# Performance work log

Hardware: AMD Instinct MI355X
Metric: run time of the kernel (lower is better)

## Reference

```python
import jax, jax.numpy as jnp
import numpy as np

NEG_SLOPE = 0.01  # F.leaky_relu default


def gcn_layer(h_in, W, b, src, dst, deg_inv_sqrt, n_nodes):
    # GCNConv: linear transform, then symmetric-normalized sum aggregation
    # with self-loops (PyG gcn_norm with add_self_loops=True).
    h = h_in @ W                                   # [N, F_out]
    norm = deg_inv_sqrt[src] * deg_inv_sqrt[dst]   # [E]
    agg = jax.ops.segment_sum(norm[:, None] * h[src], dst, num_segments=n_nodes)
    agg = agg + (deg_inv_sqrt * deg_inv_sqrt)[:, None] * h  # self-loop term (norm = 1/deg)
    return agg + b


def setup_inputs() -> dict:
    key = jax.random.key(0)
    ks = jax.random.split(key, 10)
    N, E = 100000, 3200000
    F_in, H, C = 512, 256, 64
    x = jax.random.normal(ks[0], (N, F_in), dtype=jnp.float32)
    edge_index = jax.random.randint(ks[1], (2, E), 0, N, dtype=jnp.int32)
    dims = [(F_in, H), (H, H), (H, H), (H, C)]
    params = {}
    for i, (fi, fo) in enumerate(dims):
        scale = (1.0 / fi) ** 0.5
        params[f"W{i}"] = jax.random.normal(ks[2 + i], (fi, fo), dtype=jnp.float32) * scale
        params[f"b{i}"] = jnp.zeros((fo,), dtype=jnp.float32)
    return {"x": x, "edge_index": edge_index, **params}


def reference(x, edge_index, W0, b0, W1, b1, W2, b2, W3, b3):
    N = x.shape[0]
    src, dst = edge_index[0], edge_index[1]
    # degree including self-loop (edge weights all 1)
    deg = jax.ops.segment_sum(jnp.ones_like(src, dtype=x.dtype), dst, num_segments=N) + 1.0
    deg_inv_sqrt = jax.lax.rsqrt(deg)
    Ws = [W0, W1, W2, W3]
    bs = [b0, b1, b2, b3]
    h = x
    for i in range(4):
        h = gcn_layer(h, Ws[i], bs[i], src, dst, deg_inv_sqrt, N)
        if i != 3:
            h = jax.nn.leaky_relu(h, NEG_SLOPE)
    return jax.nn.softmax(h, axis=1)
```

## Files before the change

kernel.cpp:

```cpp
#include <hip/hip_runtime.h>
#include <hip/hip_fp16.h>


#define NEG_SLOPE 0.01f

typedef __attribute__((ext_vector_type(8))) _Float16 f16x8;
typedef __attribute__((ext_vector_type(4))) float f32x4;

__device__ inline f16x8 f16x8_zero() {
    f16x8 v;
#pragma unroll
    for (int q = 0; q < 8; ++q) v[q] = (_Float16)0.f;
    return v;
}

__global__ void k_degree(const int* __restrict__ dst, int* __restrict__ cnt, int E) {
    int i = blockIdx.x * 256 + threadIdx.x;
    if (i < E) atomicAdd(&cnt[dst[i]], 1);
}

__global__ void k_dis(const int* __restrict__ cnt, float* __restrict__ dis, int N) {
    int i = blockIdx.x * 256 + threadIdx.x;
    if (i < N) dis[i] = rsqrtf((float)cnt[i] + 1.0f);
}

__global__ void k_scan1(const int* __restrict__ cnt, int* __restrict__ excl,
                        int* __restrict__ partials, int n) {
    __shared__ int tmp[1024];
    int tid = threadIdx.x;
    int i = blockIdx.x * 1024 + tid;
    int v = (i < n) ? cnt[i] : 0;
    tmp[tid] = v;
    __syncthreads();
    for (int off = 1; off < 1024; off <<= 1) {
        int t = (tid >= off) ? tmp[tid - off] : 0;
        __syncthreads();
        tmp[tid] += t;
        __syncthreads();
    }
    if (i < n) excl[i] = tmp[tid] - v;
    if (tid == 1023) partials[blockIdx.x] = tmp[tid];
}

__global__ void k_scan2(int* __restrict__ partials, int n) {
    __shared__ int tmp[1024];
    int tid = threadIdx.x;
    int v = (tid < n) ? partials[tid] : 0;
    tmp[tid] = v;
    __syncthreads();
    for (int off = 1; off < 1024; off <<= 1) {
        int t = (tid >= off) ? tmp[tid - off] : 0;
        __syncthreads();
        tmp[tid] += t;
        __syncthreads();
    }
    if (tid < n) partials[tid] = tmp[tid] - v;
}

__global__ void k_scan3(int* __restrict__ row_ptr, const int* __restrict__ partials,
                        int* __restrict__ fill_ptr, int n, int E) {
    int i = blockIdx.x * 256 + threadIdx.x;
    if (i < n) {
        int v = row_ptr[i] + partials[i >> 10];
        row_ptr[i] = v;
        fill_ptr[i] = v;
    }
    if (i == n) row_ptr[n] = E;
}

__global__ void k_fill(const int* __restrict__ src, const int* __restrict__ dst,
                       int* __restrict__ fill_ptr, int* __restrict__ csr, int E) {
    int i = blockIdx.x * 256 + threadIdx.x;
    if (i < E) {
        int s = src[i], d = dst[i];
        int p = atomicAdd(&fill_ptr[d], 1);
        csr[p] = s;
    }
}

__global__ void k_convW(const float* __restrict__ W, _Float16* __restrict__ Wt,
                        int K, int Nf) {
    int gid = blockIdx.x * 256 + threadIdx.x;
    if (gid < K * Nf) {
        int n = gid / K, k = gid - n * K;
        Wt[gid] = (_Float16)W[(size_t)k * Nf + n];
    }
}

template <int BN, bool A_HALF, bool OUT_HALF>
__global__ __launch_bounds__(256) void k_gemm_mfma(const void* __restrict__ Ap,
                                                   const _Float16* __restrict__ Bt,
                                                   void* __restrict__ Cp,
                                                   const float* __restrict__ rowscale,
                                                   int M, int K, int Nf) {
    constexpr int BM = 128, BK = 32;
    constexpr int WAVES_N = (BN == 128) ? 2 : 1;
    constexpr int WAVES_M = 4 / WAVES_N;
    constexpr int WM = BM / (WAVES_M * 16);
    constexpr int WN = BN / (WAVES_N * 16);
    constexpr int LDK = BK + 8;
    __shared__ _Float16 As[BM][LDK];
    __shared__ _Float16 Bs[BN][LDK];

    const int tid = threadIdx.x;
    const int ln = tid & 63, wv = tid >> 6;
    const int wm = wv / WAVES_N, wn = wv % WAVES_N;
    const int rowq = wm * WM * 16, colq = wn * WN * 16;
    const int rowBase = blockIdx.x * BM;
    const int colBase = blockIdx.y * BN;
    const int l15 = ln & 15, lq = ln >> 4;

    f32x4 acc[WM][WN];
#pragma unroll
    for (int i = 0; i < WM; ++i)
#pragma unroll
        for (int j = 0; j < WN; ++j) {
            acc[i][j][0] = 0.f; acc[i][j][1] = 0.f;
            acc[i][j][2] = 0.f; acc[i][j][3] = 0.f;
        }

    constexpr int ASL2 = (BM * BK / 8) / 256;
    constexpr int BSL2 = (BN * BK / 8) / 256;

    for (int kt = 0; kt < K; kt += BK) {
        f16x8 aL[ASL2];
        float4 aF[ASL2][2];
#pragma unroll
        for (int s2 = 0; s2 < ASL2; ++s2) {
            int s = tid + s2 * 256;
            int r = s >> 2, k0 = (s & 3) * 8;
            int gr = rowBase + r;
            if constexpr (A_HALF) {
                aL[s2] = (gr < M)
                    ? *(const f16x8*)((const _Float16*)Ap + (size_t)gr * K + kt + k0)
                    : f16x8_zero();
            } else {
                if (gr < M) {
                    const float* ap = (const float*)Ap + (size_t)gr * K + kt + k0;
                    aF[s2][0] = *(const float4*)ap;
                    aF[s2][1] = *(const float4*)(ap + 4);
                } else {
                    aF[s2][0] = make_float4(0.f, 0.f, 0.f, 0.f);
                    aF[s2][1] = make_float4(0.f, 0.f, 0.f, 0.f);
                }
            }
        }
        f16x8 bL[BSL2];
#pragma unroll
        for (int s2 = 0; s2 < BSL2; ++s2) {
            int s = tid + s2 * 256;
            int n = s >> 2, k0 = (s & 3) * 8;
            bL[s2] = *(const f16x8*)&Bt[(size_t)(colBase + n) * K + kt + k0];
        }
        __syncthreads();
#pragma unroll
        for (int s2 = 0; s2 < ASL2; ++s2) {
            int s = tid + s2 * 256;
            int r = s >> 2, k0 = (s & 3) * 8;
            if constexpr (A_HALF) {
                *(f16x8*)&As[r][k0] = aL[s2];
            } else {
                f16x8 h;
                h[0] = (_Float16)aF[s2][0].x; h[1] = (_Float16)aF[s2][0].y;
                h[2] = (_Float16)aF[s2][0].z; h[3] = (_Float16)aF[s2][0].w;
                h[4] = (_Float16)aF[s2][1].x; h[5] = (_Float16)aF[s2][1].y;
                h[6] = (_Float16)aF[s2][1].z; h[7] = (_Float16)aF[s2][1].w;
                *(f16x8*)&As[r][k0] = h;
            }
        }
#pragma unroll
        for (int s2 = 0; s2 < BSL2; ++s2) {
            int s = tid + s2 * 256;
            int n = s >> 2, k0 = (s & 3) * 8;
            *(f16x8*)&Bs[n][k0] = bL[s2];
        }
        __syncthreads();
        f16x8 af[WM], bf[WN];
#pragma unroll
        for (int i = 0; i < WM; ++i)
            af[i] = *(const f16x8*)&As[rowq + i * 16 + l15][lq * 8];
#pragma unroll
        for (int j = 0; j < WN; ++j)
            bf[j] = *(const f16x8*)&Bs[colq + j * 16 + l15][lq * 8];
#pragma unroll
        for (int i = 0; i < WM; ++i)
#pragma unroll
            for (int j = 0; j < WN; ++j)
                acc[i][j] = __builtin_amdgcn_mfma_f32_16x16x32_f16(af[i], bf[j],
                                                                   acc[i][j], 0, 0, 0);
    }

#pragma unroll
    for (int i = 0; i < WM; ++i) {
#pragma unroll
        for (int r = 0; r < 4; ++r) {
            int row = rowBase + rowq + i * 16 + lq * 4 + r;
            if (row < M) {
                float rs = rowscale[row];
#pragma unroll
                for (int j = 0; j < WN; ++j) {
                    int col = colBase + colq + j * 16 + l15;
                    float v = rs * acc[i][j][r];
                    if constexpr (OUT_HALF)
                        ((_Float16*)Cp)[(size_t)row * Nf + col] = (_Float16)v;
                    else
                        ((float*)Cp)[(size_t)row * Nf + col] = v;
                }
            }
        }
    }
}

__global__ __launch_bounds__(256) void k_agg256_h(const float2* __restrict__ H2,
                                                  const int* __restrict__ row_ptr,
                                                  const int* __restrict__ csr,
                                                  const float* __restrict__ dis,
                                                  const float* __restrict__ bias,
                                                  _Float16* __restrict__ out, int N) {
    int wave = threadIdx.x >> 6;
    int lane = threadIdx.x & 63;
    int node = blockIdx.x * 4 + wave;
    if (node >= N) return;
    int beg = row_ptr[node], end = row_ptr[node + 1];
    float ax = 0.f, ay = 0.f, az = 0.f, aw = 0.f;

    int e = beg;
    for (; e + 8 <= end; e += 8) {
        int msrc = csr[e + (lane & 7)];
#pragma unroll
        for (int j = 0; j < 8; ++j) {
            int s = __shfl(msrc, j);
            float2 raw = H2[(size_t)s * 64 + lane];
            float2 f0 = __half22float2(*(const __half2*)&raw.x);
            float2 f1 = __half22float2(*(const __half2*)&raw.y);
            ax += f0.x; ay += f0.y; az += f1.x; aw += f1.y;
        }
    }
    if (e < end) {
        int idx = e + (lane & 7);
        int msrc = csr[idx < end ? idx : end - 1];
        int n = end - e;
#pragma unroll
        for (int j = 0; j < 8; ++j) {
            if (j < n) {
                int s = __shfl(msrc, j);
                float2 raw = H2[(size_t)s * 64 + lane];
                float2 f0 = __half22float2(*(const __half2*)&raw.x);
                float2 f1 = __half22float2(*(const __half2*)&raw.y);
                ax += f0.x; ay += f0.y; az += f1.x; aw += f1.y;
            }
        }
    }

    float di = dis[node];
    float2 raws = H2[(size_t)node * 64 + lane];
    float2 s0 = __half22float2(*(const __half2*)&raws.x);
    float2 s1 = __half22float2(*(const __half2*)&raws.y);
    float4 b  = ((const float4*)bias)[lane];
    float rx = fmaf(di, ax + s0.x, b.x);
    float ry = fmaf(di, ay + s0.y, b.y);
    float rz = fmaf(di, az + s1.x, b.z);
    float rw = fmaf(di, aw + s1.y, b.w);
    rx = rx > 0.f ? rx : NEG_SLOPE * rx;
    ry = ry > 0.f ? ry : NEG_SLOPE * ry;
    rz = rz > 0.f ? rz : NEG_SLOPE * rz;
    rw = rw > 0.f ? rw : NEG_SLOPE * rw;
    _Float16 hh[4] = {(_Float16)rx, (_Float16)ry, (_Float16)rz, (_Float16)rw};
    *(float2*)&out[(size_t)node * 256 + lane * 4] = *(float2*)hh;
}

__global__ __launch_bounds__(256) void k_agg64_softmax(const _Float16* __restrict__ H,
                                                       const int* __restrict__ row_ptr,
                                                       const int* __restrict__ csr,
                                                       const float* __restrict__ dis,
                                                       const float* __restrict__ bias,
                                                       float* __restrict__ out, int N) {
    int wave = threadIdx.x >> 6;
    int lane = threadIdx.x & 63;
    int node = blockIdx.x * 4 + wave;
    if (node >= N) return;
    int beg = row_ptr[node], end = row_ptr[node + 1];
    float acc = 0.f;

    int e = beg;
    for (; e + 8 <= end; e += 8) {
        int msrc = csr[e + (lane & 7)];
#pragma unroll
        for (int j = 0; j < 8; ++j) {
            int s = __shfl(msrc, j);
            acc += (float)H[(size_t)s * 64 + lane];
        }
    }
    if (e < end) {
        int idx = e + (lane & 7);
        int msrc = csr[idx < end ? idx : end - 1];
        int n = end - e;
#pragma unroll
        for (int j = 0; j < 8; ++j) {
            if (j < n) {
                int s = __shfl(msrc, j);
                acc += (float)H[(size_t)s * 64 + lane];
            }
        }
    }

    float di = dis[node];
    float v = fmaf(di, acc + (float)H[(size_t)node * 64 + lane], bias[lane]);
    float m = v;
#pragma unroll
    for (int off = 32; off; off >>= 1) m = fmaxf(m, __shfl_xor(m, off));
    float ex = __expf(v - m);
    float s = ex;
#pragma unroll
    for (int off = 32; off; off >>= 1) s += __shfl_xor(s, off);
    out[(size_t)node * 64 + lane] = ex / s;
}

extern "C" void kernel_launch(void* const* d_in, const int* in_sizes, int n_in,
                              void* d_out, int out_size, void* d_ws, size_t ws_size,
                              hipStream_t stream) {
    const float* x  = (const float*)d_in[0];
    const int*   ei = (const int*)d_in[1];
    const float* W0 = (const float*)d_in[2];
    const float* b0 = (const float*)d_in[3];
    const float* W1 = (const float*)d_in[4];
    const float* b1 = (const float*)d_in[5];
    const float* W2 = (const float*)d_in[6];
    const float* b2 = (const float*)d_in[7];
    const float* W3 = (const float*)d_in[8];
    const float* b3 = (const float*)d_in[9];

    const int N = in_sizes[0] / 512;
    const int E = in_sizes[1] / 2;
    const int* src = ei;
    const int* dst = ei + E;

    auto align256 = [](size_t v) { return (v + 255) & ~(size_t)255; };
    char* w = (char*)d_ws;
    _Float16* hA = (_Float16*)w;     w += align256((size_t)N * 256 * 4);
    _Float16* hB = (_Float16*)w;     w += align256((size_t)N * 256 * 4);
    int*   csr = (int*)w;            w += align256((size_t)E * 4);
    int*   cnt = (int*)w;            w += align256((size_t)N * 4);
    float* dis = (float*)w;          w += align256((size_t)N * 4);
    int*   row_ptr = (int*)w;        w += align256((size_t)(N + 1) * 4);
    int*   fill_ptr = (int*)w;       w += align256((size_t)N * 4);
    int*   partials = (int*)w;       w += align256((size_t)1024 * 4);
    _Float16* Wt0 = (_Float16*)w;    w += align256((size_t)256 * 512 * 2);
    _Float16* Wt1 = (_Float16*)w;    w += align256((size_t)256 * 256 * 2);
    _Float16* Wt2 = (_Float16*)w;    w += align256((size_t)256 * 256 * 2);
    _Float16* Wt3 = (_Float16*)w;    w += align256((size_t)64 * 256 * 2);
    (void)ws_size; (void)n_in; (void)out_size;

    const int nchunks = (N + 1023) / 1024;

    hipMemsetAsync(cnt, 0, (size_t)N * 4, stream);
    k_degree<<<(E + 255) / 256, 256, 0, stream>>>(dst, cnt, E);
    k_dis<<<(N + 255) / 256, 256, 0, stream>>>(cnt, dis, N);
    k_scan1<<<nchunks, 1024, 0, stream>>>(cnt, row_ptr, partials, N);
    k_scan2<<<1, 1024, 0, stream>>>(partials, nchunks);
    k_scan3<<<(N + 1 + 255) / 256, 256, 0, stream>>>(row_ptr, partials, fill_ptr, N, E);
    k_fill<<<(E + 255) / 256, 256, 0, stream>>>(src, dst, fill_ptr, csr, E);

    k_convW<<<(512 * 256 + 255) / 256, 256, 0, stream>>>(W0, Wt0, 512, 256);
    k_convW<<<(256 * 256 + 255) / 256, 256, 0, stream>>>(W1, Wt1, 256, 256);
    k_convW<<<(256 * 256 + 255) / 256, 256, 0, stream>>>(W2, Wt2, 256, 256);
    k_convW<<<(256 * 64 + 255) / 256, 256, 0, stream>>>(W3, Wt3, 256, 64);

    const int gridM = (N + 127) / 128;
    const int nodeBlocks = (N + 3) / 4;

    k_gemm_mfma<128, false, true><<<dim3(gridM, 2), 256, 0, stream>>>(x, Wt0, hA, dis,
                                                                      N, 512, 256);
    k_agg256_h<<<nodeBlocks, 256, 0, stream>>>((const float2*)hA, row_ptr, csr, dis, b0,
                                               hB, N);
    k_gemm_mfma<128, true, true><<<dim3(gridM, 2), 256, 0, stream>>>(hB, Wt1, hA, dis,
                                                                     N, 256, 256);
    k_agg256_h<<<nodeBlocks, 256, 0, stream>>>((const float2*)hA, row_ptr, csr, dis, b1,
                                               hB, N);
    k_gemm_mfma<128, true, true><<<dim3(gridM, 2), 256, 0, stream>>>(hB, Wt2, hA, dis,
                                                                     N, 256, 256);
    k_agg256_h<<<nodeBlocks, 256, 0, stream>>>((const float2*)hA, row_ptr, csr, dis, b2,
                                               hB, N);
    k_gemm_mfma<64, true, true><<<dim3(gridM, 1), 256, 0, stream>>>(hB, Wt3, hA, dis,
                                                                    N, 256, 64);
    k_agg64_softmax<<<nodeBlocks, 256, 0, stream>>>(hA, row_ptr, csr, dis, b3,
                                                    (float*)d_out, N);
}
```

Before: 1.626 ms.

## Build CSR via two-level bucket fill to localize scatter atomics

```diff
diff --git a/kernel.cpp b/kernel.cpp
--- a/kernel.cpp
+++ b/kernel.cpp
@@ -58,23 +58,45 @@
 }
 
 __global__ void k_scan3(int* __restrict__ row_ptr, const int* __restrict__ partials,
-                        int* __restrict__ fill_ptr, int n, int E) {
+                        int n, int E) {
     int i = blockIdx.x * 256 + threadIdx.x;
-    if (i < n) {
-        int v = row_ptr[i] + partials[i >> 10];
-        row_ptr[i] = v;
-        fill_ptr[i] = v;
-    }
+    if (i < n) row_ptr[i] = row_ptr[i] + partials[i >> 10];
     if (i == n) row_ptr[n] = E;
 }
 
-__global__ void k_fill(const int* __restrict__ src, const int* __restrict__ dst,
-                       int* __restrict__ fill_ptr, int* __restrict__ csr, int E) {
+__global__ void k_init_bcur(const int* __restrict__ row_ptr, int* __restrict__ bcur,
+                            int nbuk) {
+    int b = blockIdx.x * 256 + threadIdx.x;
+    if (b < nbuk) bcur[b * 16] = row_ptr[b << 7];
+}
+
+__global__ void k_bucket_fill(const int* __restrict__ src, const int* __restrict__ dst,
+                              int* __restrict__ bcur, int* __restrict__ bpool, int E) {
     int i = blockIdx.x * 256 + threadIdx.x;
     if (i < E) {
         int s = src[i], d = dst[i];
-        int p = atomicAdd(&fill_ptr[d], 1);
-        csr[p] = s;
+        int b = d >> 7;
+        int p = atomicAdd(&bcur[b * 16], 1);
+        bpool[p] = (s << 7) | (d & 127);
+    }
+}
+
+__global__ __launch_bounds__(256) void k_place(const int* __restrict__ bpool,
+                                               const int* __restrict__ row_ptr,
+                                               int* __restrict__ csr, int N) {
+    __shared__ int cur[128];
+    int b = blockIdx.x;
+    int n0 = b << 7;
+    int nn = min(128, N - n0);
+    int tid = threadIdx.x;
+    if (tid < nn) cur[tid] = row_ptr[n0 + tid];
+    __syncthreads();
+    int lo = row_ptr[n0];
+    int hi = row_ptr[n0 + nn];
+    for (int i = lo + tid; i < hi; i += 256) {
+        int e = bpool[i];
+        int p = atomicAdd(&cur[e & 127], 1);
+        csr[p] = e >> 7;
     }
 }
 
@@ -334,16 +356,18 @@
     const int E = in_sizes[1] / 2;
     const int* src = ei;
     const int* dst = ei + E;
+    const int NBUK = (N + 127) >> 7;
 
     auto align256 = [](size_t v) { return (v + 255) & ~(size_t)255; };
     char* w = (char*)d_ws;
-    _Float16* hA = (_Float16*)w;     w += align256((size_t)N * 256 * 4);
-    _Float16* hB = (_Float16*)w;     w += align256((size_t)N * 256 * 4);
+    _Float16* hA = (_Float16*)w;     w += align256((size_t)N * 256 * 2);
+    _Float16* hB = (_Float16*)w;     w += align256((size_t)N * 256 * 2);
     int*   csr = (int*)w;            w += align256((size_t)E * 4);
+    int*   bpool = (int*)w;          w += align256((size_t)E * 4);
     int*   cnt = (int*)w;            w += align256((size_t)N * 4);
     float* dis = (float*)w;          w += align256((size_t)N * 4);
     int*   row_ptr = (int*)w;        w += align256((size_t)(N + 1) * 4);
-    int*   fill_ptr = (int*)w;       w += align256((size_t)N * 4);
+    int*   bcur = (int*)w;           w += align256((size_t)NBUK * 16 * 4);
     int*   partials = (int*)w;       w += align256((size_t)1024 * 4);
     _Float16* Wt0 = (_Float16*)w;    w += align256((size_t)256 * 512 * 2);
     _Float16* Wt1 = (_Float16*)w;    w += align256((size_t)256 * 256 * 2);
@@ -358,8 +382,10 @@
     k_dis<<<(N + 255) / 256, 256, 0, stream>>>(cnt, dis, N);
     k_scan1<<<nchunks, 1024, 0, stream>>>(cnt, row_ptr, partials, N);
     k_scan2<<<1, 1024, 0, stream>>>(partials, nchunks);
-    k_scan3<<<(N + 1 + 255) / 256, 256, 0, stream>>>(row_ptr, partials, fill_ptr, N, E);
-    k_fill<<<(E + 255) / 256, 256, 0, stream>>>(src, dst, fill_ptr, csr, E);
+    k_scan3<<<(N + 1 + 255) / 256, 256, 0, stream>>>(row_ptr, partials, N, E);
+    k_init_bcur<<<(NBUK + 255) / 256, 256, 0, stream>>>(row_ptr, bcur, NBUK);
+    k_bucket_fill<<<(E + 255) / 256, 256, 0, stream>>>(src, dst, bcur, bpool, E);
+    k_place<<<NBUK, 256, 0, stream>>>(bpool, row_ptr, csr, N);
 
     k_convW<<<(512 * 256 + 255) / 256, 256, 0, stream>>>(W0, Wt0, 512, 256);
     k_convW<<<(256 * 256 + 255) / 256, 256, 0, stream>>>(W1, Wt1, 256, 256);
```

Measured after the change: 1.530 ms. 1.06x faster.
